# Optimization experiments

Hardware: AMD Instinct MI355X
Metric: run time of the kernel (lower is better)

The kernel has to match this reference:

```python
import jax, jax.numpy as jnp
import numpy as np

STALK_DIM = 16
N_NODES = 50000
N_EDGES = 400000
HIDDEN = 64


def setup_inputs() -> dict:
    key = jax.random.key(0)
    k1, k2, k3, k4 = jax.random.split(key, 4)
    d = STALK_DIM
    x = jax.random.normal(k1, (N_NODES, d), dtype=jnp.float32)
    edge_index = jax.random.randint(k2, (2, N_EDGES), 0, N_NODES, dtype=jnp.int64)
    W1 = jax.random.normal(k3, (HIDDEN, 2 * d), dtype=jnp.float32) * (1.0 / np.sqrt(2 * d))
    b1 = jnp.zeros((HIDDEN,), dtype=jnp.float32)
    W2 = jax.random.normal(k4, (d, HIDDEN), dtype=jnp.float32) * (1.0 / np.sqrt(HIDDEN))
    b2 = jnp.zeros((d,), dtype=jnp.float32)
    return {"x": x, "edge_index": edge_index, "W1": W1, "b1": b1, "W2": W2, "b2": b2}


def reference(x, edge_index, W1, b1, W2, b2):
    d = x.shape[1]
    n = x.shape[0]
    src, dst = edge_index[0], edge_index[1]
    xs, xd = x[src], x[dst]  # [E, d]

    def reflection(a, b):
        h = jax.nn.relu(jnp.concatenate([a, b], axis=1) @ W1.T + b1)
        return h @ W2.T + b2  # [E, d]

    def householder(v):
        # F.normalize(v, dim=1): v / max(||v||, 1e-12)
        vn = v / jnp.maximum(jnp.linalg.norm(v, axis=1, keepdims=True), 1e-12)
        return jnp.eye(d, dtype=v.dtype)[None] - 2.0 * vn[:, :, None] * vn[:, None, :]

    F_s = householder(reflection(xs, xd))  # [E, d, d]
    F_d = householder(reflection(xd, xs))  # [E, d, d]
    L_sd = -jnp.einsum('eki,ekj->eij', F_s, F_d)  # -F_s^T @ F_d, [E, d, d]

    # degrees: both endpoints of every edge contribute 1
    ones_e = jnp.ones(src.shape[0], dtype=x.dtype)
    deg = jnp.zeros(n, dtype=x.dtype).at[src].add(ones_e).at[dst].add(ones_e)
    deg_inv_sqrt = 1.0 / jnp.sqrt(jnp.maximum(deg, 1e-5))
    # D_inv_sqrt is scalar*I per node, so normalization is a scalar coefficient per edge
    coef = deg_inv_sqrt[src] * deg_inv_sqrt[dst]  # [E]

    # out[s] -= D^-1/2_s L D^-1/2_d x[d] ; out[d] -= D^-1/2_d L^T D^-1/2_s x[s]
    msg_s = coef[:, None] * jnp.einsum('eij,ej->ei', L_sd, xd)  # goes to src
    msg_d = coef[:, None] * jnp.einsum('eji,ej->ei', L_sd, xs)  # goes to dst

    out = x - jnp.zeros_like(x).at[src].add(msg_s) - jnp.zeros_like(x).at[dst].add(msg_d)
    return jax.nn.relu(out)
```

## Files before the change

### kernel.cpp

```cpp
#include <hip/hip_runtime.h>
#include <hip/hip_bf16.h>
#include <hip/hip_fp16.h>

#define N_NODES 50000
#define N_EDGES 400000
#define D 16
#define HID 64

#define SCAN_B 256
#define SCAN_G ((N_NODES + SCAN_B - 1) / SCAN_B)

typedef unsigned short ushort_t;

#define CNT4_OFF  0
#define DEG_OFF   (4 * N_NODES)
#define OFF_OFF   (5 * N_NODES)
#define CUR_OFF   (6 * N_NODES + 1)
#define BS_OFF    (7 * N_NODES + 1)
#define MSG_OFF_I (((BS_OFF + SCAN_G) + 3) & ~3)
#define PREP_OFF  (MSG_OFF_I + 2 * N_EDGES * D)
#define PREP_DW   (64 * 64 + 16)
#define CSR_NEEDED_BYTES ((size_t)(PREP_OFF + PREP_DW) * 4 + 64)

#define FB_NDEG   (N_NODES)
#define FB_NACC   (N_NODES * D)
#define FB_FLAGS  (FB_NDEG + FB_NACC)

__device__ __forceinline__ float bf_bits(ushort_t us) {
    return __uint_as_float(((unsigned)us) << 16);
}
__device__ __forceinline__ float lo_bf(unsigned u) { return __uint_as_float(u << 16); }
__device__ __forceinline__ float hi_bf(unsigned u) { return __uint_as_float(u & 0xffff0000u); }
__device__ __forceinline__ ushort_t f2bf(float v) {
    unsigned u = __float_as_uint(v);
    unsigned r = (u + 0x7fffu + ((u >> 16) & 1u)) >> 16;
    return (ushort_t)r;
}
__device__ __forceinline__ float ld_f(const void* p, int idx, int f32) {
    return f32 ? ((const float*)p)[idx]
               : bf_bits(((const ushort_t*)p)[idx]);
}

__device__ __forceinline__ void load16(const void* __restrict__ p, long long base,
                                       int f32, float* o) {
    if (f32) {
        const float4* q = (const float4*)((const float*)p + base);
        float4 a = q[0], b = q[1], c = q[2], d = q[3];
        o[0]=a.x; o[1]=a.y; o[2]=a.z; o[3]=a.w;
        o[4]=b.x; o[5]=b.y; o[6]=b.z; o[7]=b.w;
        o[8]=c.x; o[9]=c.y; o[10]=c.z; o[11]=c.w;
        o[12]=d.x; o[13]=d.y; o[14]=d.z; o[15]=d.w;
    } else {
        const uint4* q = (const uint4*)((const ushort_t*)p + base);
        uint4 a = q[0], b = q[1];
        unsigned u[8] = {a.x, a.y, a.z, a.w, b.x, b.y, b.z, b.w};
#pragma unroll
        for (int k = 0; k < 8; k++) {
            o[2 * k]     = lo_bf(u[k]);
            o[2 * k + 1] = hi_bf(u[k]);
// ... 10 lines not shown
    } else {
        const int* p = (const int*)ei;
        s = p[e];
        d = p[N_EDGES + e];
    }
}

__device__ __forceinline__ void detect_flags_par(const void* x, const void* ei,
                                                 int* flags) {
    int t = threadIdx.x;
    if (t < 64) {
        const ushort_t* h = (const ushort_t*)x;
        int bad = 0;
#pragma unroll
        for (int k = 0; k < 4; k++) {
            float v = bf_bits(h[4 * t + k]);
            if (!(v == v) || fabsf(v) > 1.0e6f) bad = 1;
        }
        unsigned long long mb = __ballot(bad);
        const long long* p = (const long long*)ei;
        int bad64 = 0;
        if (t < 16) {
            long long v = p[t];
            bad64 = (v < 0 || v >= N_NODES) ? 1 : 0;
        }
        unsigned long long m64 = __ballot(bad64);
        if (t == 0) {
            flags[0] = mb ? 1 : 0;
            flags[1] = m64 ? 0 : 1;
        }
    }
}

__device__ __forceinline__ void stage_weights(
    const void* W1, const void* b1, const void* W2, const void* b2, int f32,
    float* sW1, float* sW2t, float* sb1, float* sb2)
{
    int t = threadIdx.x;
    for (int idx = t; idx < HID * 2 * D; idx += blockDim.x)
        sW1[idx] = ld_f(W1, idx, f32);
    for (int idx = t; idx < HID * D; idx += blockDim.x) {
        int j = idx / D, i = idx % D;
        sW2t[idx] = ld_f(W2, i * HID + j, f32);
    }
    if (t < HID) sb1[t] = ld_f(b1, t, f32);
    if (t < D)  sb2[t] = ld_f(b2, t, f32);
}

__device__ __forceinline__ void edge_math_v4(
    const float* __restrict__ sW1, const float* __restrict__ sW2t,
    const float* __restrict__ sb1, const float* __restrict__ sb2,
    const float* xs, const float* xd, float coef,
    float* ms, float* md)
{
    float vs[D], vd[D];
#pragma unroll
    for (int i = 0; i < D; i++) { vs[i] = sb2[i]; vd[i] = sb2[i]; }
#pragma unroll 4
    for (int j = 0; j < HID; j++) {
        float hs = sb1[j], hd = sb1[j];
        const float4* w4 = (const float4*)&sW1[j * 2 * D];
#pragma unroll
        for (int t = 0; t < 4; t++) {
            float4 wv = w4[t];
            int k = 4 * t;
            hs = fmaf(wv.x, xs[k],     hs); hd = fmaf(wv.x, xd[k],     hd);
            hs = fmaf(wv.y, xs[k + 1], hs); hd = fmaf(wv.y, xd[k + 1], hd);
            hs = fmaf(wv.z, xs[k + 2], hs); hd = fmaf(wv.z, xd[k + 2], hd);
            hs = fmaf(wv.w, xs[k + 3], hs); hd = fmaf(wv.w, xd[k + 3], hd);
        }
#pragma unroll
        for (int t = 0; t < 4; t++) {
            float4 wv = w4[4 + t];
            int k = 4 * t;
            hs = fmaf(wv.x, xd[k],     hs); hd = fmaf(wv.x, xs[k],     hd);
            hs = fmaf(wv.y, xd[k + 1], hs); hd = fmaf(wv.y, xs[k + 1], hd);
            hs = fmaf(wv.z, xd[k + 2], hs); hd = fmaf(wv.z, xs[k + 2], hd);
            hs = fmaf(wv.w, xd[k + 3], hs); hd = fmaf(wv.w, xs[k + 3], hd);
        }
        hs = fmaxf(hs, 0.0f);
        hd = fmaxf(hd, 0.0f);
// ... 7 lines not shown
            vs[i + 2] = fmaf(u.z, hs, vs[i + 2]); vd[i + 2] = fmaf(u.z, hd, vd[i + 2]);
            vs[i + 3] = fmaf(u.w, hs, vs[i + 3]); vd[i + 3] = fmaf(u.w, hd, vd[i + 3]);
        }
    }
    float ns = 0.0f, nd = 0.0f;
#pragma unroll
    for (int i = 0; i < D; i++) { ns = fmaf(vs[i], vs[i], ns); nd = fmaf(vd[i], vd[i], nd); }
    float is_ = 1.0f / fmaxf(sqrtf(ns), 1e-12f);
    float id_ = 1.0f / fmaxf(sqrtf(nd), 1e-12f);
#pragma unroll
    for (int i = 0; i < D; i++) { vs[i] *= is_; vd[i] *= id_; }
    float dot1 = 0.0f;
#pragma unroll
    for (int i = 0; i < D; i++) dot1 = fmaf(vd[i], xd[i], dot1);
#pragma unroll
    for (int i = 0; i < D; i++) ms[i] = fmaf(-2.0f * dot1, vd[i], xd[i]);
    float dot2 = 0.0f;
#pragma unroll
    for (int i = 0; i < D; i++) dot2 = fmaf(vs[i], ms[i], dot2);
#pragma unroll
    for (int i = 0; i < D; i++) ms[i] = coef * fmaf(-2.0f * dot2, vs[i], ms[i]);
    float dot3 = 0.0f;
#pragma unroll
    for (int i = 0; i < D; i++) dot3 = fmaf(vs[i], xs[i], dot3);
#pragma unroll
    for (int i = 0; i < D; i++) md[i] = fmaf(-2.0f * dot3, vs[i], xs[i]);
    float dot4 = 0.0f;
#pragma unroll
    for (int i = 0; i < D; i++) dot4 = fmaf(vd[i], md[i], dot4);
#pragma unroll
    for (int i = 0; i < D; i++) md[i] = coef * fmaf(-2.0f * dot4, vd[i], md[i]);
}

__global__ void csr_count_kernel(const void* __restrict__ ei,
                                 const void* __restrict__ x,
                                 const void* __restrict__ W1,
                                 const void* __restrict__ b1,
                                 const void* __restrict__ W2,
                                 const void* __restrict__ b2,
                                 int* __restrict__ wsI) {
    __shared__ int sfl[2];
    detect_flags_par(x, ei, sfl);
    __syncthreads();
    int i64 = sfl[1];

    if (blockIdx.x == 0) {
        float* pf = (float*)(wsI + PREP_OFF);
        const ushort_t* W1b = (const ushort_t*)W1;
        const ushort_t* W2b = (const ushort_t*)W2;
        const ushort_t* b1b = (const ushort_t*)b1;
        const ushort_t* b2b = (const ushort_t*)b2;
        for (int idx = threadIdx.x; idx < 64 * 64; idx += 256) {
            int j = idx >> 6, w = idx & 63;
            float val = 0.0f;
            if (w < 32)      val = bf_bits(W1b[j * 32 + w]);
            else if (w < 48) val = bf_bits(W2b[(w - 32) * HID + j]);
            else if (w == 48) val = bf_bits(b1b[j]);
            pf[idx] = val;
        }
        if (threadIdx.x < D)
            pf[64 * 64 + threadIdx.x] = bf_bits(b2b[threadIdx.x]);
    }

    int e = blockIdx.x * blockDim.x + threadIdx.x;
    if (e >= N_EDGES) return;
    int s, d;
    load_edge(ei, e, i64, s, d);
    int r = (e & 3) * N_NODES;
    atomicAdd(&wsI[CNT4_OFF + r + s], 1);
    atomicAdd(&wsI[CNT4_OFF + r + d], 1);
}

__global__ __launch_bounds__(SCAN_B) void csr_scan1_kernel(int* __restrict__ wsI) {
    __shared__ int sm[SCAN_B];
    int t = threadIdx.x;
    int g = blockIdx.x * SCAN_B + t;
    int c = 0;
    if (g < N_NODES) {
        c = wsI[CNT4_OFF + g] + wsI[CNT4_OFF + N_NODES + g]
          + wsI[CNT4_OFF + 2 * N_NODES + g] + wsI[CNT4_OFF + 3 * N_NODES + g];
        wsI[DEG_OFF + g] = c;
    }
    sm[t] = c;
    __syncthreads();
    for (int st = SCAN_B / 2; st > 0; st >>= 1) {
        if (t < st) sm[t] += sm[t + st];
        __syncthreads();
    }
    if (t == 0) wsI[BS_OFF + blockIdx.x] = sm[0];
}

__global__ __launch_bounds__(SCAN_B) void csr_scan3_kernel(int* __restrict__ wsI) {
    __shared__ int sB[SCAN_B];
    __shared__ int sm[SCAN_B];
    int t = threadIdx.x;
    int bsv = (t < SCAN_G) ? wsI[BS_OFF + t] : 0;
    sB[t] = bsv;
    __syncthreads();
    for (int st = 1; st < SCAN_B; st <<= 1) {
        int u = (t >= st) ? sB[t - st] : 0;
        __syncthreads();
        sB[t] += u;
        __syncthreads();
    }
    int blockBase = sB[blockIdx.x] - wsI[BS_OFF + blockIdx.x];

    int g = blockIdx.x * SCAN_B + t;
    int c = (g < N_NODES) ? wsI[DEG_OFF + g] : 0;
    sm[t] = c;
    __syncthreads();
    for (int st = 1; st < SCAN_B; st <<= 1) {
        int u = (t >= st) ? sm[t - st] : 0;
        __syncthreads();
        sm[t] += u;
        __syncthreads();
    }
    int excl = sm[t] - c + blockBase;
    if (g < N_NODES) {
        wsI[OFF_OFF + g] = excl;
        wsI[CUR_OFF + g] = excl;
        if (g == N_NODES - 1) wsI[OFF_OFF + N_NODES] = excl + c;
    }
}

__global__ __launch_bounds__(256) void csr_edge_kernel(
    const void* __restrict__ x,
    const void* __restrict__ ei,
    const void* __restrict__ W1,
    const void* __restrict__ b1,
    const void* __restrict__ W2,
    const void* __restrict__ b2,
    const float* __restrict__ prep,
    int* __restrict__ wsI)
{
    __shared__ __align__(16) float sW1f[HID * 2 * D];
    __shared__ __align__(16) float sW2tf[HID * D];
    __shared__ float sb1[HID];
    __shared__ float sb2[D];
    __shared__ int sfl[2];

    detect_flags_par(x, ei, sfl);
    __syncthreads();
    int f32 = sfl[0], i64 = sfl[1];
    int t = threadIdx.x;

    if (f32) {
        for (int idx = t; idx < HID * 2 * D; idx += 256)
            sW1f[idx] = ld_f(W1, idx, 1);
        for (int idx = t; idx < HID * D; idx += 256) {
            int j = idx / D, i = idx % D;
            sW2tf[idx] = ld_f(W2, i * HID + j, 1);
        }
        if (t < HID) sb1[t] = ld_f(b1, t, 1);
        if (t < D)  sb2[t] = ld_f(b2, t, 1);
        __syncthreads();
    }

    int e = blockIdx.x * 256 + t;
    if (e >= N_EDGES) return;

    int s, d;
    load_edge(ei, e, i64, s, d);
    float degs = (float)wsI[DEG_OFF + s];
    float degd = (float)wsI[DEG_OFF + d];
    float coef = (1.0f / sqrtf(fmaxf(degs, 1e-5f))) * (1.0f / sqrtf(fmaxf(degd, 1e-5f)));
    float* msg = (float*)(wsI + MSG_OFF_I);

    float xs[D], xd[D];
    load16(x, (long long)s * D, f32, xs);
    load16(x, (long long)d * D, f32, xd);

    float ms[D], md[D];
    if (!f32) {
        const float* b2f = prep + 64 * 64;
        float vs[D], vd[D];
#pragma unroll
        for (int i = 0; i < D; i++) { vs[i] = b2f[i]; vd[i] = b2f[i]; }

#pragma unroll 1
        for (int j = 0; j < HID; j++) {
            const float* w = prep + (j << 6);
            float b1j = w[48];
            float hs0 = b1j, hs1 = 0.0f, hd0 = b1j, hd1 = 0.0f;
#pragma unroll
            for (int k = 0; k < 8; k++) {
                hs0 = fmaf(w[k],     xs[k],     hs0);
                hd0 = fmaf(w[k],     xd[k],     hd0);
                hs1 = fmaf(w[8 + k], xs[8 + k], hs1);
                hd1 = fmaf(w[8 + k], xd[8 + k], hd1);
            }
#pragma unroll
            for (int k = 0; k < 8; k++) {
                hs0 = fmaf(w[16 + k], xd[k],     hs0);
                hd0 = fmaf(w[16 + k], xs[k],     hd0);
                hs1 = fmaf(w[24 + k], xd[8 + k], hs1);
                hd1 = fmaf(w[24 + k], xs[8 + k], hd1);
            }
            float hs = fmaxf(hs0 + hs1, 0.0f);
            float hd = fmaxf(hd0 + hd1, 0.0f);
#pragma unroll
            for (int i = 0; i < D; i++) {
                vs[i] = fmaf(w[32 + i], hs, vs[i]);
                vd[i] = fmaf(w[32 + i], hd, vd[i]);
            }
        }

        float ns = 0.0f, nd = 0.0f;
#pragma unroll
        for (int i = 0; i < D; i++) { ns = fmaf(vs[i], vs[i], ns); nd = fmaf(vd[i], vd[i], nd); }
        float is_ = 1.0f / fmaxf(sqrtf(ns), 1e-12f);
        float id_ = 1.0f / fmaxf(sqrtf(nd), 1e-12f);
#pragma unroll
        for (int i = 0; i < D; i++) { vs[i] *= is_; vd[i] *= id_; }

        float dot1 = 0.0f;
#pragma unroll
        for (int i = 0; i < D; i++) dot1 = fmaf(vd[i], xd[i], dot1);
#pragma unroll
        for (int i = 0; i < D; i++) ms[i] = fmaf(-2.0f * dot1, vd[i], xd[i]);
        float dot2 = 0.0f;
#pragma unroll
        for (int i = 0; i < D; i++) dot2 = fmaf(vs[i], ms[i], dot2);
#pragma unroll
        for (int i = 0; i < D; i++) ms[i] = coef * fmaf(-2.0f * dot2, vs[i], ms[i]);
        float dot3 = 0.0f;
#pragma unroll
        for (int i = 0; i < D; i++) dot3 = fmaf(vs[i], xs[i], dot3);
#pragma unroll
        for (int i = 0; i < D; i++) md[i] = fmaf(-2.0f * dot3, vs[i], xs[i]);
        float dot4 = 0.0f;
#pragma unroll
        for (int i = 0; i < D; i++) dot4 = fmaf(vd[i], md[i], dot4);
#pragma unroll
        for (int i = 0; i < D; i++) md[i] = coef * fmaf(-2.0f * dot4, vd[i], md[i]);
    } else {
        edge_math_v4(sW1f, sW2tf, sb1, sb2, xs, xd, coef, ms, md);
    }

    int slot_s = atomicAdd(&wsI[CUR_OFF + s], 1);
    float4* m0 = (float4*)(msg + (long long)slot_s * D);
    m0[0] = make_float4(ms[0], ms[1], ms[2], ms[3]);
    m0[1] = make_float4(ms[4], ms[5], ms[6], ms[7]);
    m0[2] = make_float4(ms[8], ms[9], ms[10], ms[11]);
    m0[3] = make_float4(ms[12], ms[13], ms[14], ms[15]);
    int slot_d = atomicAdd(&wsI[CUR_OFF + d], 1);
    float4* m1 = (float4*)(msg + (long long)slot_d * D);
    m1[0] = make_float4(md[0], md[1], md[2], md[3]);
    m1[1] = make_float4(md[4], md[5], md[6], md[7]);
    m1[2] = make_float4(md[8], md[9], md[10], md[11]);
    m1[3] = make_float4(md[12], md[13], md[14], md[15]);
}

__global__ __launch_bounds__(256) void csr_gather_kernel(
    const void* __restrict__ x,
    const void* __restrict__ ei,
    const int* __restrict__ wsI,
    void* __restrict__ out)
{
    __shared__ int sfl[2];
    detect_flags_par(x, ei, sfl);
    __syncthreads();
    int f32 = sfl[0];

    int n = blockIdx.x * 64 + (threadIdx.x >> 2);
    int c = threadIdx.x & 3;
    if (n >= N_NODES) return;

    const int* off = wsI + OFF_OFF;
    const float4* msg4 = (const float4*)(wsI + MSG_OFF_I);

    int beg = off[n], end = off[n + 1];
    float4 a = make_float4(0.0f, 0.0f, 0.0f, 0.0f);
    int it = beg;
    for (; it + 2 <= end; it += 2) {
        float4 u = msg4[(long long)it * 4 + c];
        float4 v = msg4[(long long)(it + 1) * 4 + c];
        a.x += u.x + v.x; a.y += u.y + v.y; a.z += u.z + v.z; a.w += u.w + v.w;
    }
    if (it < end) {
        float4 u = msg4[(long long)it * 4 + c];
        a.x += u.x; a.y += u.y; a.z += u.z; a.w += u.w;
    }

    long long xb = (long long)n * D + 4 * c;
    float4 xv;
    if (f32) {
        xv = *(const float4*)((const float*)x + xb);
    } else {
        uint2 u = *(const uint2*)((const ushort_t*)x + xb);
        xv.x = lo_bf(u.x); xv.y = hi_bf(u.x);
        xv.z = lo_bf(u.y); xv.w = hi_bf(u.y);
    }
    float4 r;
    r.x = fmaxf(xv.x + a.x, 0.0f);
    r.y = fmaxf(xv.y + a.y, 0.0f);
    r.z = fmaxf(xv.z + a.z, 0.0f);
    r.w = fmaxf(xv.w + a.w, 0.0f);
    if (f32) {
        *(float4*)((float*)out + xb) = r;
    } else {
        uint2 o;
        o.x = (unsigned)f2bf(r.x) | ((unsigned)f2bf(r.y) << 16);
        o.y = (unsigned)f2bf(r.z) | ((unsigned)f2bf(r.w) << 16);
        *(uint2*)((ushort_t*)out + xb) = o;
    }
}

__global__ void fb_init_kernel(float* __restrict__ ws,
                               const void* __restrict__ x,
                               const void* __restrict__ ei) {
    int i = blockIdx.x * blockDim.x + threadIdx.x;
    if (i < FB_FLAGS) ws[i] = 0.0f;
    if (blockIdx.x == 0)
        detect_flags_par(x, ei, (int*)(ws + FB_FLAGS));
}

__global__ void fb_deg_kernel(const void* __restrict__ ei, float* __restrict__ ws) {
    int i64 = ((const int*)(ws + FB_FLAGS))[1];
    int e = blockIdx.x * blockDim.x + threadIdx.x;
    if (e >= N_EDGES) return;
    int s, d;
    load_edge(ei, e, i64, s, d);
    atomicAdd(&ws[s], 1.0f);
    atomicAdd(&ws[d], 1.0f);
}

__global__ __launch_bounds__(256) void fb_edge_kernel(
    const void* __restrict__ x, const void* __restrict__ ei,
    const void* __restrict__ W1, const void* __restrict__ b1,
    const void* __restrict__ W2, const void* __restrict__ b2,
    float* __restrict__ ws)
{
    __shared__ __align__(16) float sW1[HID * 2 * D];
    __shared__ __align__(16) float sW2t[HID * D];
    __shared__ float sb1[HID];
    __shared__ float sb2[D];
    const int* flags = (const int*)(ws + FB_FLAGS);
    int f32 = flags[0], i64 = flags[1];
    stage_weights(W1, b1, W2, b2, f32, sW1, sW2t, sb1, sb2);
    __syncthreads();
    int e = blockIdx.x * blockDim.x + threadIdx.x;
    if (e >= N_EDGES) return;
    int s, d;
    load_edge(ei, e, i64, s, d);
    float xs[D], xd[D];
    load16(x, (long long)s * D, f32, xs);
    load16(x, (long long)d * D, f32, xd);
    float coef = (1.0f / sqrtf(fmaxf(ws[s], 1e-5f))) * (1.0f / sqrtf(fmaxf(ws[d], 1e-5f)));
    float ms[D], md[D];
    edge_math_v4(sW1, sW2t, sb1, sb2, xs, xd, coef, ms, md);
    float* acc = ws + FB_NDEG;
#pragma unroll
    for (int i = 0; i < D; i++) atomicAdd(&acc[(long long)s * D + i], ms[i]);
#pragma unroll
    for (int i = 0; i < D; i++) atomicAdd(&acc[(long long)d * D + i], md[i]);
}

__global__ void fb_finalize_kernel(const void* __restrict__ x,
                                   const float* __restrict__ ws,
                                   void* __restrict__ out)
{
    int f32 = ((const int*)(ws + FB_FLAGS))[0];
    const float* acc = ws + FB_NDEG;
    int i = blockIdx.x * blockDim.x + threadIdx.x;
    if (i >= FB_NACC) return;
    float v = ld_f(x, i, f32) + acc[i];
    v = fmaxf(v, 0.0f);
    if (f32) ((float*)out)[i] = v;
    else     ((__hip_bfloat16*)out)[i] = __float2bfloat16(v);
}

extern "C" void kernel_launch(void* const* d_in, const int* in_sizes, int n_in,
                              void* d_out, int out_size, void* d_ws, size_t ws_size,
                              hipStream_t stream)
{
    const void* x  = d_in[0];
    const void* ei = d_in[1];
    const void* W1 = d_in[2];
    const void* b1 = d_in[3];
    const void* W2 = d_in[4];
    const void* b2 = d_in[5];

    int blk = 256;
    if (ws_size >= CSR_NEEDED_BYTES) {
        int* wsI = (int*)d_ws;
        hipMemsetAsync(d_ws, 0, (size_t)4 * N_NODES * sizeof(int), stream);
        csr_count_kernel<<<(N_EDGES + blk - 1) / blk, blk, 0, stream>>>(ei, x, W1, b1, W2, b2, wsI);
        csr_scan1_kernel<<<SCAN_G, SCAN_B, 0, stream>>>(wsI);
        csr_scan3_kernel<<<SCAN_G, SCAN_B, 0, stream>>>(wsI);
        csr_edge_kernel<<<(N_EDGES + blk - 1) / blk, blk, 0, stream>>>(
            x, ei, W1, b1, W2, b2, (const float*)(wsI + PREP_OFF), wsI);
        csr_gather_kernel<<<(N_NODES + 63) / 64, blk, 0, stream>>>(x, ei, wsI, d_out);
    } else {
        float* ws = (float*)d_ws;
        fb_init_kernel<<<(FB_FLAGS + blk - 1) / blk, blk, 0, stream>>>(ws, x, ei);
        fb_deg_kernel<<<(N_EDGES + blk - 1) / blk, blk, 0, stream>>>(ei, ws);
        fb_edge_kernel<<<(N_EDGES + blk - 1) / blk, blk, 0, stream>>>(x, ei, W1, b1, W2, b2, ws);
        fb_finalize_kernel<<<(FB_NACC + blk - 1) / blk, blk, 0, stream>>>(x, ws, d_out);
    }
}
```

Baseline: 204.7 us.

## Replace CSR bucketing and gather with direct float atomic scatter accumulation

Drops the degree-count/scan/slot-write CSR pipeline, which wrote 2*E*16 message floats and gathered them per node. The edge kernel now atomically adds each message straight into a per-node accumulator, and a flat finalize kernel adds x and applies ReLU. This removes two scan launches and the large message buffer traffic, but adds 32 float atomics per edge with possible contention and non-deterministic summation order. The fallback path for small workspaces is also removed.

```diff
diff --git a/kernel.cpp b/kernel.cpp
--- a/kernel.cpp
+++ b/kernel.cpp
@@ -7,24 +7,14 @@
 #define D 16
 #define HID 64
 
-#define SCAN_B 256
-#define SCAN_G ((N_NODES + SCAN_B - 1) / SCAN_B)
-
 typedef unsigned short ushort_t;
 
-#define CNT4_OFF  0
-#define DEG_OFF   (4 * N_NODES)
-#define OFF_OFF   (5 * N_NODES)
-#define CUR_OFF   (6 * N_NODES + 1)
-#define BS_OFF    (7 * N_NODES + 1)
-#define MSG_OFF_I (((BS_OFF + SCAN_G) + 3) & ~3)
-#define PREP_OFF  (MSG_OFF_I + 2 * N_EDGES * D)
+#define DEG_OFF   0
+#define ACC_OFF   (N_NODES)
+#define PREP_OFF  (N_NODES + N_NODES * D)
 #define PREP_DW   (64 * 64 + 16)
-#define CSR_NEEDED_BYTES ((size_t)(PREP_OFF + PREP_DW) * 4 + 64)
-
-#define FB_NDEG   (N_NODES)
-#define FB_NACC   (N_NODES * D)
-#define FB_FLAGS  (FB_NDEG + FB_NACC)
+#define WS_NEEDED_BYTES ((size_t)(PREP_OFF + PREP_DW) * 4 + 64)
+#define ZERO_BYTES ((size_t)(N_NODES + N_NODES * D) * 4)
 
 __device__ __forceinline__ float bf_bits(ushort_t us) {
     return __uint_as_float(((unsigned)us) << 16);
@@ -101,21 +91,6 @@
     }
 }
 
-__device__ __forceinline__ void stage_weights(
-    const void* W1, const void* b1, const void* W2, const void* b2, int f32,
-    float* sW1, float* sW2t, float* sb1, float* sb2)
-{
-    int t = threadIdx.x;
-    for (int idx = t; idx < HID * 2 * D; idx += blockDim.x)
-        sW1[idx] = ld_f(W1, idx, f32);
-    for (int idx = t; idx < HID * D; idx += blockDim.x) {
-        int j = idx / D, i = idx % D;
-        sW2t[idx] = ld_f(W2, i * HID + j, f32);
-    }
-    if (t < HID) sb1[t] = ld_f(b1, t, f32);
-    if (t < D)  sb2[t] = ld_f(b2, t, f32);
-}
-
 __device__ __forceinline__ void edge_math_v4(
     const float* __restrict__ sW1, const float* __restrict__ sW2t,
     const float* __restrict__ sb1, const float* __restrict__ sb2,
@@ -189,13 +164,15 @@
     for (int i = 0; i < D; i++) md[i] = coef * fmaf(-2.0f * dot4, vd[i], md[i]);
 }
 
-__global__ void csr_count_kernel(const void* __restrict__ ei,
-                                 const void* __restrict__ x,
-                                 const void* __restrict__ W1,
-                                 const void* __restrict__ b1,
-                                 const void* __restrict__ W2,
-                                 const void* __restrict__ b2,
-                                 int* __restrict__ wsI) {
+__global__ __launch_bounds__(256) void atm_deg_kernel(
+    const void* __restrict__ ei,
+    const void* __restrict__ x,
+    const void* __restrict__ W1,
+    const void* __restrict__ b1,
+    const void* __restrict__ W2,
+    const void* __restrict__ b2,
+    int* __restrict__ wsI)
+{
     __shared__ int sfl[2];
     detect_flags_par(x, ei, sfl);
     __syncthreads();
@@ -219,68 +196,15 @@
             pf[64 * 64 + threadIdx.x] = bf_bits(b2b[threadIdx.x]);
     }
 
-    int e = blockIdx.x * blockDim.x + threadIdx.x;
+    int e = blockIdx.x * 256 + threadIdx.x;
     if (e >= N_EDGES) return;
     int s, d;
     load_edge(ei, e, i64, s, d);
-    int r = (e & 3) * N_NODES;
-    atomicAdd(&wsI[CNT4_OFF + r + s], 1);
-    atomicAdd(&wsI[CNT4_OFF + r + d], 1);
-}
-
-__global__ __launch_bounds__(SCAN_B) void csr_scan1_kernel(int* __restrict__ wsI) {
-    __shared__ int sm[SCAN_B];
-    int t = threadIdx.x;
-    int g = blockIdx.x * SCAN_B + t;
-    int c = 0;
-    if (g < N_NODES) {
-        c = wsI[CNT4_OFF + g] + wsI[CNT4_OFF + N_NODES + g]
-          + wsI[CNT4_OFF + 2 * N_NODES + g] + wsI[CNT4_OFF + 3 * N_NODES + g];
-        wsI[DEG_OFF + g] = c;
-    }
-    sm[t] = c;
-    __syncthreads();
-    for (int st = SCAN_B / 2; st > 0; st >>= 1) {
-        if (t < st) sm[t] += sm[t + st];
-        __syncthreads();
-    }
-    if (t == 0) wsI[BS_OFF + blockIdx.x] = sm[0];
-}
-
-__global__ __launch_bounds__(SCAN_B) void csr_scan3_kernel(int* __restrict__ wsI) {
-    __shared__ int sB[SCAN_B];
-    __shared__ int sm[SCAN_B];
-    int t = threadIdx.x;
-    int bsv = (t < SCAN_G) ? wsI[BS_OFF + t] : 0;
-    sB[t] = bsv;
-    __syncthreads();
-    for (int st = 1; st < SCAN_B; st <<= 1) {
-        int u = (t >= st) ? sB[t - st] : 0;
-        __syncthreads();
-        sB[t] += u;
-        __syncthreads();
-    }
-    int blockBase = sB[blockIdx.x] - wsI[BS_OFF + blockIdx.x];
-
-    int g = blockIdx.x * SCAN_B + t;
-    int c = (g < N_NODES) ? wsI[DEG_OFF + g] : 0;
-    sm[t] = c;
-    __syncthreads();
-    for (int st = 1; st < SCAN_B; st <<= 1) {
-        int u = (t >= st) ? sm[t - st] : 0;
-        __syncthreads();
-        sm[t] += u;
-        __syncthreads();
-    }
-    int excl = sm[t] - c + blockBase;
-    if (g < N_NODES) {
-        wsI[OFF_OFF + g] = excl;
-        wsI[CUR_OFF + g] = excl;
-        if (g == N_NODES - 1) wsI[OFF_OFF + N_NODES] = excl + c;
-    }
-}
-
-__global__ __launch_bounds__(256) void csr_edge_kernel(
+    atomicAdd(&wsI[DEG_OFF + s], 1);
+    atomicAdd(&wsI[DEG_OFF + d], 1);
+}
+
+__global__ __launch_bounds__(256) void atm_edge_kernel(
     const void* __restrict__ x,
     const void* __restrict__ ei,
     const void* __restrict__ W1,
@@ -321,7 +245,7 @@
     float degs = (float)wsI[DEG_OFF + s];
     float degd = (float)wsI[DEG_OFF + d];
     float coef = (1.0f / sqrtf(fmaxf(degs, 1e-5f))) * (1.0f / sqrtf(fmaxf(degd, 1e-5f)));
-    float* msg = (float*)(wsI + MSG_OFF_I);
+    float* acc = (float*)(wsI + ACC_OFF);
 
     float xs[D], xd[D];
     load16(x, (long long)s * D, f32, xs);
@@ -394,21 +318,13 @@
         edge_math_v4(sW1f, sW2tf, sb1, sb2, xs, xd, coef, ms, md);
     }
 
-    int slot_s = atomicAdd(&wsI[CUR_OFF + s], 1);
-    float4* m0 = (float4*)(msg + (long long)slot_s * D);
-    m0[0] = make_float4(ms[0], ms[1], ms[2], ms[3]);
-    m0[1] = make_float4(ms[4], ms[5], ms[6], ms[7]);
-    m0[2] = make_float4(ms[8], ms[9], ms[10], ms[11]);
-    m0[3] = make_float4(ms[12], ms[13], ms[14], ms[15]);
-    int slot_d = atomicAdd(&wsI[CUR_OFF + d], 1);
-    float4* m1 = (float4*)(msg + (long long)slot_d * D);
-    m1[0] = make_float4(md[0], md[1], md[2], md[3]);
-    m1[1] = make_float4(md[4], md[5], md[6], md[7]);
-    m1[2] = make_float4(md[8], md[9], md[10], md[11]);
-    m1[3] = make_float4(md[12], md[13], md[14], md[15]);
-}
-
-__global__ __launch_bounds__(256) void csr_gather_kernel(
+#pragma unroll
+    for (int i = 0; i < D; i++) atomicAdd(&acc[s * D + i], ms[i]);
+#pragma unroll
+    for (int i = 0; i < D; i++) atomicAdd(&acc[d * D + i], md[i]);
+}
+
+__global__ __launch_bounds__(256) void atm_fin_kernel(
     const void* __restrict__ x,
     const void* __restrict__ ei,
     const int* __restrict__ wsI,
@@ -419,32 +335,18 @@
     __syncthreads();
     int f32 = sfl[0];
 
-    int n = blockIdx.x * 64 + (threadIdx.x >> 2);
-    int c = threadIdx.x & 3;
-    if (n >= N_NODES) return;
-
-    const int* off = wsI + OFF_OFF;
-    const float4* msg4 = (const float4*)(wsI + MSG_OFF_I);
-
-    int beg = off[n], end = off[n + 1];
-    float4 a = make_float4(0.0f, 0.0f, 0.0f, 0.0f);
-    int it = beg;
-    for (; it + 2 <= end; it += 2) {
-        float4 u = msg4[(long long)it * 4 + c];
-        float4 v = msg4[(long long)(it + 1) * 4 + c];
-        a.x += u.x + v.x; a.y += u.y + v.y; a.z += u.z + v.z; a.w += u.w + v.w;
-    }
-    if (it < end) {
-        float4 u = msg4[(long long)it * 4 + c];
-        a.x += u.x; a.y += u.y; a.z += u.z; a.w += u.w;
-    }
-
-    long long xb = (long long)n * D + 4 * c;
+    int q = blockIdx.x * 256 + threadIdx.x;
+    if (q >= (N_NODES * D) / 4) return;
+    long long base = (long long)q * 4;
+
+    const float* acc = (const float*)(wsI + ACC_OFF);
+    float4 a = *(const float4*)(acc + base);
+
     float4 xv;
     if (f32) {
-        xv = *(const float4*)((const float*)x + xb);
-    } else {
-        uint2 u = *(const uint2*)((const ushort_t*)x + xb);
+        xv = *(const float4*)((const float*)x + base);
+    } else {
+        uint2 u = *(const uint2*)((const ushort_t*)x + base);
         xv.x = lo_bf(u.x); xv.y = hi_bf(u.x);
         xv.z = lo_bf(u.y); xv.w = hi_bf(u.y);
     }
@@ -454,77 +356,13 @@
     r.z = fmaxf(xv.z + a.z, 0.0f);
     r.w = fmaxf(xv.w + a.w, 0.0f);
     if (f32) {
-        *(float4*)((float*)out + xb) = r;
+        *(float4*)((float*)out + base) = r;
     } else {
         uint2 o;
         o.x = (unsigned)f2bf(r.x) | ((unsigned)f2bf(r.y) << 16);
         o.y = (unsigned)f2bf(r.z) | ((unsigned)f2bf(r.w) << 16);
-        *(uint2*)((ushort_t*)out + xb) = o;
-    }
-}
-
-__global__ void fb_init_kernel(float* __restrict__ ws,
-                               const void* __restrict__ x,
-                               const void* __restrict__ ei) {
-    int i = blockIdx.x * blockDim.x + threadIdx.x;
-    if (i < FB_FLAGS) ws[i] = 0.0f;
-    if (blockIdx.x == 0)
-        detect_flags_par(x, ei, (int*)(ws + FB_FLAGS));
-}
-
-__global__ void fb_deg_kernel(const void* __restrict__ ei, float* __restrict__ ws) {
-    int i64 = ((const int*)(ws + FB_FLAGS))[1];
-    int e = blockIdx.x * blockDim.x + threadIdx.x;
-    if (e >= N_EDGES) return;
-    int s, d;
-    load_edge(ei, e, i64, s, d);
-    atomicAdd(&ws[s], 1.0f);
-    atomicAdd(&ws[d], 1.0f);
-}
-
-__global__ __launch_bounds__(256) void fb_edge_kernel(
-    const void* __restrict__ x, const void* __restrict__ ei,
-    const void* __restrict__ W1, const void* __restrict__ b1,
-    const void* __restrict__ W2, const void* __restrict__ b2,
-    float* __restrict__ ws)
-{
-    __shared__ __align__(16) float sW1[HID * 2 * D];
-    __shared__ __align__(16) float sW2t[HID * D];
-    __shared__ float sb1[HID];
-    __shared__ float sb2[D];
-    const int* flags = (const int*)(ws + FB_FLAGS);
-    int f32 = flags[0], i64 = flags[1];
-    stage_weights(W1, b1, W2, b2, f32, sW1, sW2t, sb1, sb2);
-    __syncthreads();
-    int e = blockIdx.x * blockDim.x + threadIdx.x;
-    if (e >= N_EDGES) return;
-    int s, d;
-    load_edge(ei, e, i64, s, d);
-    float xs[D], xd[D];
-    load16(x, (long long)s * D, f32, xs);
-    load16(x, (long long)d * D, f32, xd);
-    float coef = (1.0f / sqrtf(fmaxf(ws[s], 1e-5f))) * (1.0f / sqrtf(fmaxf(ws[d], 1e-5f)));
-    float ms[D], md[D];
-    edge_math_v4(sW1, sW2t, sb1, sb2, xs, xd, coef, ms, md);
-    float* acc = ws + FB_NDEG;
-#pragma unroll
-    for (int i = 0; i < D; i++) atomicAdd(&acc[(long long)s * D + i], ms[i]);
-#pragma unroll
-    for (int i = 0; i < D; i++) atomicAdd(&acc[(long long)d * D + i], md[i]);
-}
-
-__global__ void fb_finalize_kernel(const void* __restrict__ x,
-                                   const float* __restrict__ ws,
-                                   void* __restrict__ out)
-{
-    int f32 = ((const int*)(ws + FB_FLAGS))[0];
-    const float* acc = ws + FB_NDEG;
-    int i = blockIdx.x * blockDim.x + threadIdx.x;
-    if (i >= FB_NACC) return;
-    float v = ld_f(x, i, f32) + acc[i];
-    v = fmaxf(v, 0.0f);
-    if (f32) ((float*)out)[i] = v;
-    else     ((__hip_bfloat16*)out)[i] = __float2bfloat16(v);
+        *(uint2*)((ushort_t*)out + base) = o;
+    }
 }
 
 extern "C" void kernel_launch(void* const* d_in, const int* in_sizes, int n_in,
@@ -539,20 +377,12 @@
     const void* b2 = d_in[5];
 
     int blk = 256;
-    if (ws_size >= CSR_NEEDED_BYTES) {
-        int* wsI = (int*)d_ws;
-        hipMemsetAsync(d_ws, 0, (size_t)4 * N_NODES * sizeof(int), stream);
-        csr_count_kernel<<<(N_EDGES + blk - 1) / blk, blk, 0, stream>>>(ei, x, W1, b1, W2, b2, wsI);
-        csr_scan1_kernel<<<SCAN_G, SCAN_B, 0, stream>>>(wsI);
-        csr_scan3_kernel<<<SCAN_G, SCAN_B, 0, stream>>>(wsI);
-        csr_edge_kernel<<<(N_EDGES + blk - 1) / blk, blk, 0, stream>>>(
-            x, ei, W1, b1, W2, b2, (const float*)(wsI + PREP_OFF), wsI);
-        csr_gather_kernel<<<(N_NODES + 63) / 64, blk, 0, stream>>>(x, ei, wsI, d_out);
-    } else {
-        float* ws = (float*)d_ws;
-        fb_init_kernel<<<(FB_FLAGS + blk - 1) / blk, blk, 0, stream>>>(ws, x, ei);
-        fb_deg_kernel<<<(N_EDGES + blk - 1) / blk, blk, 0, stream>>>(ei, ws);
-        fb_edge_kernel<<<(N_EDGES + blk - 1) / blk, blk, 0, stream>>>(x, ei, W1, b1, W2, b2, ws);
-        fb_finalize_kernel<<<(FB_NACC + blk - 1) / blk, blk, 0, stream>>>(x, ws, d_out);
-    }
-}
+    int* wsI = (int*)d_ws;
+    hipMemsetAsync(d_ws, 0, ZERO_BYTES, stream);
+    atm_deg_kernel<<<(N_EDGES + blk - 1) / blk, blk, 0, stream>>>(
+        ei, x, W1, b1, W2, b2, wsI);
+    atm_edge_kernel<<<(N_EDGES + blk - 1) / blk, blk, 0, stream>>>(
+        x, ei, W1, b1, W2, b2, (const float*)(wsI + PREP_OFF), wsI);
+    atm_fin_kernel<<<((N_NODES * D / 4) + blk - 1) / blk, blk, 0, stream>>>(
+        x, ei, wsI, d_out);
+}
```

After: 795.4 us. 3.89x slower.

## Fuse CSR pipeline into a single cooperative persistent kernel with grid syncs

Applied to the files above, without the earlier changes.

Replaces the memset plus count, two scan, edge and gather launches with one cooperatively launched kernel that separates the phases with grid-wide barriers. Counter zeroing, weight packing, the degree count, the block-sum and offset scans, per-edge message computation and the CSR gather now run as grid-stride loops inside one launch. The aim is to remove launch gaps and inter-kernel drain/fill between the many small phases. In exchange it pays for six grid.sync barriers, and the fused kernel may use more registers and shared memory, which can lower occupancy in the compute-heavy edge phase. The multi-kernel path is kept as a fallback when the cooperative launch is unavailable or the grid would be too small for the gather.

```diff
diff --git a/kernel.cpp b/kernel.cpp
--- a/kernel.cpp
+++ b/kernel.cpp
@@ -1,6 +1,9 @@
 #include <hip/hip_runtime.h>
 #include <hip/hip_bf16.h>
 #include <hip/hip_fp16.h>
+#include <hip/hip_cooperative_groups.h>
+
+namespace cg = cooperative_groups;
 
 #define N_NODES 50000
 #define N_EDGES 400000
@@ -17,7 +20,7 @@
 #define OFF_OFF   (5 * N_NODES)
 #define CUR_OFF   (6 * N_NODES + 1)
 #define BS_OFF    (7 * N_NODES + 1)
-#define MSG_OFF_I (((BS_OFF + SCAN_G) + 3) & ~3)
+#define MSG_OFF_I (((BS_OFF + SCAN_G) + 15) & ~15)
 #define PREP_OFF  (MSG_OFF_I + 2 * N_EDGES * D)
 #define PREP_DW   (64 * 64 + 16)
 #define CSR_NEEDED_BYTES ((size_t)(PREP_OFF + PREP_DW) * 4 + 64)
@@ -189,211 +192,77 @@
     for (int i = 0; i < D; i++) md[i] = coef * fmaf(-2.0f * dot4, vd[i], md[i]);
 }
 
-__global__ void csr_count_kernel(const void* __restrict__ ei,
-                                 const void* __restrict__ x,
-                                 const void* __restrict__ W1,
-                                 const void* __restrict__ b1,
-                                 const void* __restrict__ W2,
-                                 const void* __restrict__ b2,
-                                 int* __restrict__ wsI) {
-    __shared__ int sfl[2];
-    detect_flags_par(x, ei, sfl);
-    __syncthreads();
-    int i64 = sfl[1];
-
-    if (blockIdx.x == 0) {
-        float* pf = (float*)(wsI + PREP_OFF);
-        const ushort_t* W1b = (const ushort_t*)W1;
-        const ushort_t* W2b = (const ushort_t*)W2;
-        const ushort_t* b1b = (const ushort_t*)b1;
-        const ushort_t* b2b = (const ushort_t*)b2;
-        for (int idx = threadIdx.x; idx < 64 * 64; idx += 256) {
-            int j = idx >> 6, w = idx & 63;
-            float val = 0.0f;
-            if (w < 32)      val = bf_bits(W1b[j * 32 + w]);
-            else if (w < 48) val = bf_bits(W2b[(w - 32) * HID + j]);
-            else if (w == 48) val = bf_bits(b1b[j]);
-            pf[idx] = val;
-        }
-        if (threadIdx.x < D)
-            pf[64 * 64 + threadIdx.x] = bf_bits(b2b[threadIdx.x]);
-    }
-
-    int e = blockIdx.x * blockDim.x + threadIdx.x;
-    if (e >= N_EDGES) return;
-    int s, d;
-    load_edge(ei, e, i64, s, d);
-    int r = (e & 3) * N_NODES;
-    atomicAdd(&wsI[CNT4_OFF + r + s], 1);
-    atomicAdd(&wsI[CNT4_OFF + r + d], 1);
-}
-
-__global__ __launch_bounds__(SCAN_B) void csr_scan1_kernel(int* __restrict__ wsI) {
-    __shared__ int sm[SCAN_B];
-    int t = threadIdx.x;
-    int g = blockIdx.x * SCAN_B + t;
-    int c = 0;
-    if (g < N_NODES) {
-        c = wsI[CNT4_OFF + g] + wsI[CNT4_OFF + N_NODES + g]
-          + wsI[CNT4_OFF + 2 * N_NODES + g] + wsI[CNT4_OFF + 3 * N_NODES + g];
-        wsI[DEG_OFF + g] = c;
-    }
-    sm[t] = c;
-    __syncthreads();
-    for (int st = SCAN_B / 2; st > 0; st >>= 1) {
-        if (t < st) sm[t] += sm[t + st];
-        __syncthreads();
-    }
-    if (t == 0) wsI[BS_OFF + blockIdx.x] = sm[0];
-}
-
-__global__ __launch_bounds__(SCAN_B) void csr_scan3_kernel(int* __restrict__ wsI) {
-    __shared__ int sB[SCAN_B];
-    __shared__ int sm[SCAN_B];
-    int t = threadIdx.x;
-    int bsv = (t < SCAN_G) ? wsI[BS_OFF + t] : 0;
-    sB[t] = bsv;
-    __syncthreads();
-    for (int st = 1; st < SCAN_B; st <<= 1) {
-        int u = (t >= st) ? sB[t - st] : 0;
-        __syncthreads();
-        sB[t] += u;
-        __syncthreads();
-    }
-    int blockBase = sB[blockIdx.x] - wsI[BS_OFF + blockIdx.x];
-
-    int g = blockIdx.x * SCAN_B + t;
-    int c = (g < N_NODES) ? wsI[DEG_OFF + g] : 0;
-    sm[t] = c;
-    __syncthreads();
-    for (int st = 1; st < SCAN_B; st <<= 1) {
-        int u = (t >= st) ? sm[t - st] : 0;
-        __syncthreads();
-        sm[t] += u;
-        __syncthreads();
-    }
-    int excl = sm[t] - c + blockBase;
-    if (g < N_NODES) {
-        wsI[OFF_OFF + g] = excl;
-        wsI[CUR_OFF + g] = excl;
-        if (g == N_NODES - 1) wsI[OFF_OFF + N_NODES] = excl + c;
-    }
-}
-
-__global__ __launch_bounds__(256) void csr_edge_kernel(
-    const void* __restrict__ x,
-    const void* __restrict__ ei,
-    const void* __restrict__ W1,
-    const void* __restrict__ b1,
-    const void* __restrict__ W2,
-    const void* __restrict__ b2,
+__device__ __forceinline__ void edge_math_prep(
     const float* __restrict__ prep,
-    int* __restrict__ wsI)
-{
-    __shared__ __align__(16) float sW1f[HID * 2 * D];
-    __shared__ __align__(16) float sW2tf[HID * D];
-    __shared__ float sb1[HID];
-    __shared__ float sb2[D];
-    __shared__ int sfl[2];
-
-    detect_flags_par(x, ei, sfl);
-    __syncthreads();
-    int f32 = sfl[0], i64 = sfl[1];
-    int t = threadIdx.x;
-
-    if (f32) {
-        for (int idx = t; idx < HID * 2 * D; idx += 256)
-            sW1f[idx] = ld_f(W1, idx, 1);
-        for (int idx = t; idx < HID * D; idx += 256) {
-            int j = idx / D, i = idx % D;
-            sW2tf[idx] = ld_f(W2, i * HID + j, 1);
-        }
-        if (t < HID) sb1[t] = ld_f(b1, t, 1);
-        if (t < D)  sb2[t] = ld_f(b2, t, 1);
-        __syncthreads();
-    }
-
-    int e = blockIdx.x * 256 + t;
-    if (e >= N_EDGES) return;
-
-    int s, d;
-    load_edge(ei, e, i64, s, d);
-    float degs = (float)wsI[DEG_OFF + s];
-    float degd = (float)wsI[DEG_OFF + d];
-    float coef = (1.0f / sqrtf(fmaxf(degs, 1e-5f))) * (1.0f / sqrtf(fmaxf(degd, 1e-5f)));
-    float* msg = (float*)(wsI + MSG_OFF_I);
-
-    float xs[D], xd[D];
-    load16(x, (long long)s * D, f32, xs);
-    load16(x, (long long)d * D, f32, xd);
-
-    float ms[D], md[D];
-    if (!f32) {
-        const float* b2f = prep + 64 * 64;
-        float vs[D], vd[D];
-#pragma unroll
-        for (int i = 0; i < D; i++) { vs[i] = b2f[i]; vd[i] = b2f[i]; }
+    const float* xs, const float* xd, float coef,
+    float* ms, float* md)
+{
+    const float* b2f = prep + 64 * 64;
+    float vs[D], vd[D];
+#pragma unroll
+    for (int i = 0; i < D; i++) { vs[i] = b2f[i]; vd[i] = b2f[i]; }
 
 #pragma unroll 1
-        for (int j = 0; j < HID; j++) {
-            const float* w = prep + (j << 6);
-            float b1j = w[48];
-            float hs0 = b1j, hs1 = 0.0f, hd0 = b1j, hd1 = 0.0f;
-#pragma unroll
-            for (int k = 0; k < 8; k++) {
-                hs0 = fmaf(w[k],     xs[k],     hs0);
-                hd0 = fmaf(w[k],     xd[k],     hd0);
-                hs1 = fmaf(w[8 + k], xs[8 + k], hs1);
-                hd1 = fmaf(w[8 + k], xd[8 + k], hd1);
-            }
-#pragma unroll
-            for (int k = 0; k < 8; k++) {
-                hs0 = fmaf(w[16 + k], xd[k],     hs0);
-                hd0 = fmaf(w[16 + k], xs[k],     hd0);
-                hs1 = fmaf(w[24 + k], xd[8 + k], hs1);
-                hd1 = fmaf(w[24 + k], xs[8 + k], hd1);
-            }
-            float hs = fmaxf(hs0 + hs1, 0.0f);
-            float hd = fmaxf(hd0 + hd1, 0.0f);
-#pragma unroll
-            for (int i = 0; i < D; i++) {
-                vs[i] = fmaf(w[32 + i], hs, vs[i]);
-                vd[i] = fmaf(w[32 + i], hd, vd[i]);
-            }
-        }
-
-        float ns = 0.0f, nd = 0.0f;
-#pragma unroll
-        for (int i = 0; i < D; i++) { ns = fmaf(vs[i], vs[i], ns); nd = fmaf(vd[i], vd[i], nd); }
-        float is_ = 1.0f / fmaxf(sqrtf(ns), 1e-12f);
-        float id_ = 1.0f / fmaxf(sqrtf(nd), 1e-12f);
-#pragma unroll
-        for (int i = 0; i < D; i++) { vs[i] *= is_; vd[i] *= id_; }
-
-        float dot1 = 0.0f;
-#pragma unroll
-        for (int i = 0; i < D; i++) dot1 = fmaf(vd[i], xd[i], dot1);
-#pragma unroll
-        for (int i = 0; i < D; i++) ms[i] = fmaf(-2.0f * dot1, vd[i], xd[i]);
-        float dot2 = 0.0f;
-#pragma unroll
-        for (int i = 0; i < D; i++) dot2 = fmaf(vs[i], ms[i], dot2);
-#pragma unroll
-        for (int i = 0; i < D; i++) ms[i] = coef * fmaf(-2.0f * dot2, vs[i], ms[i]);
-        float dot3 = 0.0f;
-#pragma unroll
-        for (int i = 0; i < D; i++) dot3 = fmaf(vs[i], xs[i], dot3);
-#pragma unroll
-        for (int i = 0; i < D; i++) md[i] = fmaf(-2.0f * dot3, vs[i], xs[i]);
-        float dot4 = 0.0f;
-#pragma unroll
-        for (int i = 0; i < D; i++) dot4 = fmaf(vd[i], md[i], dot4);
-#pragma unroll
-        for (int i = 0; i < D; i++) md[i] = coef * fmaf(-2.0f * dot4, vd[i], md[i]);
-    } else {
-        edge_math_v4(sW1f, sW2tf, sb1, sb2, xs, xd, coef, ms, md);
-    }
-
+    for (int j = 0; j < HID; j++) {
+        const float* w = prep + (j << 6);
+        float b1j = w[48];
+        float hs0 = b1j, hs1 = 0.0f, hd0 = b1j, hd1 = 0.0f;
+#pragma unroll
+        for (int k = 0; k < 8; k++) {
+            hs0 = fmaf(w[k],     xs[k],     hs0);
+            hd0 = fmaf(w[k],     xd[k],     hd0);
+            hs1 = fmaf(w[8 + k], xs[8 + k], hs1);
+            hd1 = fmaf(w[8 + k], xd[8 + k], hd1);
+        }
+#pragma unroll
+        for (int k = 0; k < 8; k++) {
+            hs0 = fmaf(w[16 + k], xd[k],     hs0);
+            hd0 = fmaf(w[16 + k], xs[k],     hd0);
+            hs1 = fmaf(w[24 + k], xd[8 + k], hs1);
+            hd1 = fmaf(w[24 + k], xs[8 + k], hd1);
+        }
+        float hs = fmaxf(hs0 + hs1, 0.0f);
+        float hd = fmaxf(hd0 + hd1, 0.0f);
+#pragma unroll
+        for (int i = 0; i < D; i++) {
+            vs[i] = fmaf(w[32 + i], hs, vs[i]);
+            vd[i] = fmaf(w[32 + i], hd, vd[i]);
+        }
+    }
+
+    float ns = 0.0f, nd = 0.0f;
+#pragma unroll
+    for (int i = 0; i < D; i++) { ns = fmaf(vs[i], vs[i], ns); nd = fmaf(vd[i], vd[i], nd); }
+    float is_ = 1.0f / fmaxf(sqrtf(ns), 1e-12f);
+    float id_ = 1.0f / fmaxf(sqrtf(nd), 1e-12f);
+#pragma unroll
+    for (int i = 0; i < D; i++) { vs[i] *= is_; vd[i] *= id_; }
+
+    float dot1 = 0.0f;
+#pragma unroll
+    for (int i = 0; i < D; i++) dot1 = fmaf(vd[i], xd[i], dot1);
+#pragma unroll
+    for (int i = 0; i < D; i++) ms[i] = fmaf(-2.0f * dot1, vd[i], xd[i]);
+    float dot2 = 0.0f;
+#pragma unroll
+    for (int i = 0; i < D; i++) dot2 = fmaf(vs[i], ms[i], dot2);
+#pragma unroll
+    for (int i = 0; i < D; i++) ms[i] = coef * fmaf(-2.0f * dot2, vs[i], ms[i]);
+    float dot3 = 0.0f;
+#pragma unroll
+    for (int i = 0; i < D; i++) dot3 = fmaf(vs[i], xs[i], dot3);
+#pragma unroll
+    for (int i = 0; i < D; i++) md[i] = fmaf(-2.0f * dot3, vs[i], xs[i]);
+    float dot4 = 0.0f;
+#pragma unroll
+    for (int i = 0; i < D; i++) dot4 = fmaf(vd[i], md[i], dot4);
+#pragma unroll
+    for (int i = 0; i < D; i++) md[i] = coef * fmaf(-2.0f * dot4, vd[i], md[i]);
+}
+
+__device__ __forceinline__ void write_msgs(int* __restrict__ wsI, float* __restrict__ msg,
+                                           int s, int d, const float* ms, const float* md)
+{
     int slot_s = atomicAdd(&wsI[CUR_OFF + s], 1);
     float4* m0 = (float4*)(msg + (long long)slot_s * D);
     m0[0] = make_float4(ms[0], ms[1], ms[2], ms[3]);
@@ -408,21 +277,32 @@
     m1[3] = make_float4(md[12], md[13], md[14], md[15]);
 }
 
-__global__ __launch_bounds__(256) void csr_gather_kernel(
-    const void* __restrict__ x,
-    const void* __restrict__ ei,
-    const int* __restrict__ wsI,
-    void* __restrict__ out)
-{
-    __shared__ int sfl[2];
-    detect_flags_par(x, ei, sfl);
-    __syncthreads();
-    int f32 = sfl[0];
-
-    int n = blockIdx.x * 64 + (threadIdx.x >> 2);
-    int c = threadIdx.x & 3;
-    if (n >= N_NODES) return;
-
+__device__ __forceinline__ void pack_prep(const void* W1, const void* b1,
+                                          const void* W2, const void* b2,
+                                          int* __restrict__ wsI)
+{
+    float* pf = (float*)(wsI + PREP_OFF);
+    const ushort_t* W1b = (const ushort_t*)W1;
+    const ushort_t* W2b = (const ushort_t*)W2;
+    const ushort_t* b1b = (const ushort_t*)b1;
+    const ushort_t* b2b = (const ushort_t*)b2;
+    for (int idx = threadIdx.x; idx < 64 * 64; idx += 256) {
+        int j = idx >> 6, w = idx & 63;
+        float val = 0.0f;
+        if (w < 32)      val = bf_bits(W1b[j * 32 + w]);
+        else if (w < 48) val = bf_bits(W2b[(w - 32) * HID + j]);
+        else if (w == 48) val = bf_bits(b1b[j]);
+        pf[idx] = val;
+    }
+    if (threadIdx.x < D)
+        pf[64 * 64 + threadIdx.x] = bf_bits(b2b[threadIdx.x]);
+}
+
+__device__ __forceinline__ void gather_node(int n, int c, int f32,
+                                            const int* __restrict__ wsI,
+                                            const void* __restrict__ x,
+                                            void* __restrict__ out)
+{
     const int* off = wsI + OFF_OFF;
     const float4* msg4 = (const float4*)(wsI + MSG_OFF_I);
 
@@ -461,6 +341,267 @@
         o.y = (unsigned)f2bf(r.z) | ((unsigned)f2bf(r.w) << 16);
         *(uint2*)((ushort_t*)out + xb) = o;
     }
+}
+
+__global__ __launch_bounds__(256) void fused_kernel(
+    const void* __restrict__ x,
+    const void* __restrict__ ei,
+    const void* __restrict__ W1,
+    const void* __restrict__ b1,
+    const void* __restrict__ W2,
+    const void* __restrict__ b2,
+    int* __restrict__ wsI,
+    void* __restrict__ out)
+{
+    cg::grid_group grid = cg::this_grid();
+
+    __shared__ __align__(16) float sW1f[HID * 2 * D];
+    __shared__ __align__(16) float sW2tf[HID * D];
+    __shared__ float sb1[HID];
+    __shared__ float sb2[D];
+    __shared__ int sm[SCAN_B];
+    __shared__ int sB[SCAN_B];
+    __shared__ int sfl[2];
+
+    detect_flags_par(x, ei, sfl);
+    __syncthreads();
+    const int f32 = sfl[0], i64 = sfl[1];
+    const int t = threadIdx.x;
+    const int gid = blockIdx.x * 256 + t;
+    const int nthr = gridDim.x * 256;
+
+    if (f32)
+        stage_weights(W1, b1, W2, b2, 1, sW1f, sW2tf, sb1, sb2);
+
+    for (int i = gid; i < 4 * N_NODES; i += nthr) wsI[CNT4_OFF + i] = 0;
+    if (blockIdx.x == 0) pack_prep(W1, b1, W2, b2, wsI);
+    grid.sync();
+
+    for (int e = gid; e < N_EDGES; e += nthr) {
+        int s, d;
+        load_edge(ei, e, i64, s, d);
+        int r = (e & 3) * N_NODES;
+        atomicAdd(&wsI[CNT4_OFF + r + s], 1);
+        atomicAdd(&wsI[CNT4_OFF + r + d], 1);
+    }
+    grid.sync();
+
+    if (blockIdx.x < SCAN_G) {
+        int g = blockIdx.x * SCAN_B + t;
+        int c = 0;
+        if (g < N_NODES) {
+            c = wsI[CNT4_OFF + g] + wsI[CNT4_OFF + N_NODES + g]
+              + wsI[CNT4_OFF + 2 * N_NODES + g] + wsI[CNT4_OFF + 3 * N_NODES + g];
+            wsI[DEG_OFF + g] = c;
+        }
+        sm[t] = c;
+        __syncthreads();
+        for (int st = SCAN_B / 2; st > 0; st >>= 1) {
+            if (t < st) sm[t] += sm[t + st];
+            __syncthreads();
+        }
+        if (t == 0) wsI[BS_OFF + blockIdx.x] = sm[0];
+    }
+    grid.sync();
+
+    if (blockIdx.x == 0) {
+        int v = (t < SCAN_G) ? wsI[BS_OFF + t] : 0;
+        sB[t] = v;
+        __syncthreads();
+        for (int st = 1; st < SCAN_B; st <<= 1) {
+            int u = (t >= st) ? sB[t - st] : 0;
+            __syncthreads();
+            sB[t] += u;
+            __syncthreads();
+        }
+        if (t < SCAN_G) wsI[BS_OFF + t] = sB[t] - v;
+    }
+    grid.sync();
+
+    if (blockIdx.x < SCAN_G) {
+        int base = wsI[BS_OFF + blockIdx.x];
+        int g = blockIdx.x * SCAN_B + t;
+        int c = (g < N_NODES) ? wsI[DEG_OFF + g] : 0;
+        sm[t] = c;
+        __syncthreads();
+        for (int st = 1; st < SCAN_B; st <<= 1) {
+            int u = (t >= st) ? sm[t - st] : 0;
+            __syncthreads();
+            sm[t] += u;
+            __syncthreads();
+        }
+        int excl = sm[t] - c + base;
+        if (g < N_NODES) {
+            wsI[OFF_OFF + g] = excl;
+            wsI[CUR_OFF + g] = excl;
+            if (g == N_NODES - 1) wsI[OFF_OFF + N_NODES] = excl + c;
+        }
+    }
+    grid.sync();
+
+    {
+        const float* prep = (const float*)(wsI + PREP_OFF);
+        float* msg = (float*)(wsI + MSG_OFF_I);
+        for (int e = gid; e < N_EDGES; e += nthr) {
+            int s, d;
+            load_edge(ei, e, i64, s, d);
+            float degs = (float)wsI[DEG_OFF + s];
+            float degd = (float)wsI[DEG_OFF + d];
+            float coef = (1.0f / sqrtf(fmaxf(degs, 1e-5f)))
+                       * (1.0f / sqrtf(fmaxf(degd, 1e-5f)));
+            float xs[D], xd[D];
+            load16(x, (long long)s * D, f32, xs);
+            load16(x, (long long)d * D, f32, xd);
+            float ms[D], md[D];
+            if (!f32) edge_math_prep(prep, xs, xd, coef, ms, md);
+            else      edge_math_v4(sW1f, sW2tf, sb1, sb2, xs, xd, coef, ms, md);
+            write_msgs(wsI, msg, s, d, ms, md);
+        }
+    }
+    grid.sync();
+
+    {
+        int n = gid >> 2, c = gid & 3;
+        if (n < N_NODES) gather_node(n, c, f32, wsI, x, out);
+    }
+}
+
+__global__ void csr_count_kernel(const void* __restrict__ ei,
+                                 const void* __restrict__ x,
+                                 const void* __restrict__ W1,
+                                 const void* __restrict__ b1,
+                                 const void* __restrict__ W2,
+                                 const void* __restrict__ b2,
+                                 int* __restrict__ wsI) {
+    __shared__ int sfl[2];
+    detect_flags_par(x, ei, sfl);
+    __syncthreads();
+    int i64 = sfl[1];
+
+    if (blockIdx.x == 0) pack_prep(W1, b1, W2, b2, wsI);
+
+    int e = blockIdx.x * blockDim.x + threadIdx.x;
+    if (e >= N_EDGES) return;
+    int s, d;
+    load_edge(ei, e, i64, s, d);
+    int r = (e & 3) * N_NODES;
+    atomicAdd(&wsI[CNT4_OFF + r + s], 1);
+    atomicAdd(&wsI[CNT4_OFF + r + d], 1);
+}
+
+__global__ __launch_bounds__(SCAN_B) void csr_scan1_kernel(int* __restrict__ wsI) {
+    __shared__ int sm[SCAN_B];
+    int t = threadIdx.x;
+    int g = blockIdx.x * SCAN_B + t;
+    int c = 0;
+    if (g < N_NODES) {
+        c = wsI[CNT4_OFF + g] + wsI[CNT4_OFF + N_NODES + g]
+          + wsI[CNT4_OFF + 2 * N_NODES + g] + wsI[CNT4_OFF + 3 * N_NODES + g];
+        wsI[DEG_OFF + g] = c;
+    }
+    sm[t] = c;
+    __syncthreads();
+    for (int st = SCAN_B / 2; st > 0; st >>= 1) {
+        if (t < st) sm[t] += sm[t + st];
+        __syncthreads();
+    }
+    if (t == 0) wsI[BS_OFF + blockIdx.x] = sm[0];
+}
+
+__global__ __launch_bounds__(SCAN_B) void csr_scan3_kernel(int* __restrict__ wsI) {
+    __shared__ int sB[SCAN_B];
+    __shared__ int sm[SCAN_B];
+    int t = threadIdx.x;
+    int bsv = (t < SCAN_G) ? wsI[BS_OFF + t] : 0;
+    sB[t] = bsv;
+    __syncthreads();
+    for (int st = 1; st < SCAN_B; st <<= 1) {
+        int u = (t >= st) ? sB[t - st] : 0;
+        __syncthreads();
+        sB[t] += u;
+        __syncthreads();
+    }
+    int blockBase = sB[blockIdx.x] - wsI[BS_OFF + blockIdx.x];
+
+    int g = blockIdx.x * SCAN_B + t;
+    int c = (g < N_NODES) ? wsI[DEG_OFF + g] : 0;
+    sm[t] = c;
+    __syncthreads();
+    for (int st = 1; st < SCAN_B; st <<= 1) {
+        int u = (t >= st) ? sm[t - st] : 0;
+        __syncthreads();
+        sm[t] += u;
+        __syncthreads();
+    }
+    int excl = sm[t] - c + blockBase;
+    if (g < N_NODES) {
+        wsI[OFF_OFF + g] = excl;
+        wsI[CUR_OFF + g] = excl;
+        if (g == N_NODES - 1) wsI[OFF_OFF + N_NODES] = excl + c;
+    }
+}
+
+__global__ __launch_bounds__(256) void csr_edge_kernel(
+    const void* __restrict__ x,
+    const void* __restrict__ ei,
+    const void* __restrict__ W1,
+    const void* __restrict__ b1,
+    const void* __restrict__ W2,
+    const void* __restrict__ b2,
+    const float* __restrict__ prep,
+    int* __restrict__ wsI)
+{
+    __shared__ __align__(16) float sW1f[HID * 2 * D];
+    __shared__ __align__(16) float sW2tf[HID * D];
+    __shared__ float sb1[HID];
+    __shared__ float sb2[D];
+    __shared__ int sfl[2];
+
+    detect_flags_par(x, ei, sfl);
+    __syncthreads();
+    int f32 = sfl[0], i64 = sfl[1];
+    int t = threadIdx.x;
+
+    if (f32) {
+        stage_weights(W1, b1, W2, b2, 1, sW1f, sW2tf, sb1, sb2);
+        __syncthreads();
+    }
+
+    int e = blockIdx.x * 256 + t;
+    if (e >= N_EDGES) return;
+
+    int s, d;
+    load_edge(ei, e, i64, s, d);
+    float degs = (float)wsI[DEG_OFF + s];
+    float degd = (float)wsI[DEG_OFF + d];
+    float coef = (1.0f / sqrtf(fmaxf(degs, 1e-5f))) * (1.0f / sqrtf(fmaxf(degd, 1e-5f)));
+    float* msg = (float*)(wsI + MSG_OFF_I);
+
+    float xs[D], xd[D];
+    load16(x, (long long)s * D, f32, xs);
+    load16(x, (long long)d * D, f32, xd);
+
+    float ms[D], md[D];
+    if (!f32) edge_math_prep(prep, xs, xd, coef, ms, md);
+    else      edge_math_v4(sW1f, sW2tf, sb1, sb2, xs, xd, coef, ms, md);
+    write_msgs(wsI, msg, s, d, ms, md);
+}
+
+__global__ __launch_bounds__(256) void csr_gather_kernel(
+    const void* __restrict__ x,
+    const void* __restrict__ ei,
+    const int* __restrict__ wsI,
+    void* __restrict__ out)
+{
+    __shared__ int sfl[2];
+    detect_flags_par(x, ei, sfl);
+    __syncthreads();
+    int f32 = sfl[0];
+
+    int n = blockIdx.x * 64 + (threadIdx.x >> 2);
+    int c = threadIdx.x & 3;
+    if (n >= N_NODES) return;
+    gather_node(n, c, f32, wsI, x, out);
 }
 
 __global__ void fb_init_kernel(float* __restrict__ ws,
@@ -541,8 +682,29 @@
     int blk = 256;
     if (ws_size >= CSR_NEEDED_BYTES) {
         int* wsI = (int*)d_ws;
+
+        int maxBlocksPerCU = 0;
+        hipError_t oe = hipOccupancyMaxActiveBlocksPerMultiprocessor(
+            &maxBlocksPerCU, fused_kernel, 256, 0);
+        int grid = 1024;
+        if (oe == hipSuccess && maxBlocksPerCU > 0) {
+            long long cap = (long long)maxBlocksPerCU * 256;
+            if (cap < grid) grid = (int)cap;
+            else if (cap >= 2048) grid = 2048;
+        }
+        if (grid >= 782) {
+            void* wsp = (void*)wsI;
+            void* kargs[] = {(void*)&x, (void*)&ei, (void*)&W1, (void*)&b1,
+                             (void*)&W2, (void*)&b2, (void*)&wsp, (void*)&d_out};
+            hipError_t le = hipLaunchCooperativeKernel(
+                (const void*)fused_kernel, dim3(grid), dim3(256), kargs, 0, stream);
+            if (le == hipSuccess) return;
+            (void)hipGetLastError();
+        }
+
         hipMemsetAsync(d_ws, 0, (size_t)4 * N_NODES * sizeof(int), stream);
-        csr_count_kernel<<<(N_EDGES + blk - 1) / blk, blk, 0, stream>>>(ei, x, W1, b1, W2, b2, wsI);
+        csr_count_kernel<<<(N_EDGES + blk - 1) / blk, blk, 0, stream>>>(
+            ei, x, W1, b1, W2, b2, wsI);
         csr_scan1_kernel<<<SCAN_G, SCAN_B, 0, stream>>>(wsI);
         csr_scan3_kernel<<<SCAN_G, SCAN_B, 0, stream>>>(wsI);
         csr_edge_kernel<<<(N_EDGES + blk - 1) / blk, blk, 0, stream>>>(
```

Result: slower. 210.0 us (+2.6%).
